# Performance work log

Measured on AMD Instinct MI355X. Metric: run time of the kernel, lower is better.

The kernel has to match this reference:

```python
import jax, jax.numpy as jnp
import numpy as np
from jax import lax

B, L, C = 8, 1024, 256
H = 8  # num_heads
EPS = 1e-5


def _conv_bn(img, w, gamma, beta):
    # img: [B, C_in, h, w]; w: [C_out, C_in, 3, 3]; 3x3 conv, stride 1, pad 1, no bias
    out = lax.conv_general_dilated(img, w, window_strides=(1, 1),
                                   padding=[(1, 1), (1, 1)],
                                   dimension_numbers=('NCHW', 'OIHW', 'NCHW'))
    # BatchNorm2d in train mode: per-channel batch stats over (B, h, w), biased var
    mu = out.mean(axis=(0, 2, 3), keepdims=True)
    var = out.var(axis=(0, 2, 3), keepdims=True)
    out = (out - mu) * lax.rsqrt(var + EPS)
    out = out * gamma[None, :, None, None] + beta[None, :, None, None]
    b, c, hh, ww = out.shape
    return out.reshape(b, c, hh * ww).transpose(0, 2, 1)  # b (h w) c


def setup_inputs() -> dict:
    key = jax.random.key(0)
    ks = jax.random.split(key, 10)
    s = 0.02
    inp = {
        'x': jax.random.normal(ks[0], (B, L, C), jnp.float32),
        'y': jax.random.normal(ks[1], (B, L, C), jnp.float32),
        'h': 32,
        'w': 32,
        'conv_q_w': jax.random.normal(ks[2], (C, C, 3, 3), jnp.float32) * s,
        'bn_q_g': jnp.ones((C,), jnp.float32),
        'bn_q_b': jnp.zeros((C,), jnp.float32),
        'conv_k_w': jax.random.normal(ks[3], (C, C, 3, 3), jnp.float32) * s,
        'bn_k_g': jnp.ones((C,), jnp.float32),
        'bn_k_b': jnp.zeros((C,), jnp.float32),
        'conv_v_w': jax.random.normal(ks[4], (C, C, 3, 3), jnp.float32) * s,
        'bn_v_g': jnp.ones((C,), jnp.float32),
        'bn_v_b': jnp.zeros((C,), jnp.float32),
        'Wq': jax.random.normal(ks[5], (C, C), jnp.float32) * s,
        'Wk': jax.random.normal(ks[6], (C, C), jnp.float32) * s,
        'Wv': jax.random.normal(ks[7], (C, C), jnp.float32) * s,
        'Wo': jax.random.normal(ks[8], (C, C), jnp.float32) * s,
        'bo': jnp.zeros((C,), jnp.float32),
    }
    return inp


def reference(x, y, h, w,
              conv_q_w, bn_q_g, bn_q_b,
              conv_k_w, bn_k_g, bn_k_b,
              conv_v_w, bn_v_g, bn_v_b,
              Wq, Wk, Wv, Wo, bo):
    b, t, c = x.shape
    x_img = x.transpose(0, 2, 1).reshape(b, c, h, w)
    y_img = y.transpose(0, 2, 1).reshape(b, c, h, w)

    q = _conv_bn(x_img, conv_q_w, bn_q_g, bn_q_b)  # [B, L, C]
    k = _conv_bn(y_img, conv_k_w, bn_k_g, bn_k_b)
    v = _conv_bn(y_img, conv_v_w, bn_v_g, bn_v_b)

    d = c // H
    # Linear (no bias) then split heads: b t (h d) -> b h t d
    q = (q @ Wq.T).reshape(b, -1, H, d).transpose(0, 2, 1, 3)
    k = (k @ Wk.T).reshape(b, -1, H, d).transpose(0, 2, 1, 3)
    v = (v @ Wv.T).reshape(b, -1, H, d).transpose(0, 2, 1, 3)

    scale = c ** (-0.5)  # NOTE: original scales by dim_q**-0.5, not head_dim
    attn = jax.nn.softmax(jnp.einsum('bhlk,bhtk->bhlt', q, k) * scale, axis=-1)
    out = jnp.einsum('bhlt,bhtv->bhlv', attn, v)
    out = out.transpose(0, 2, 1, 3).reshape(b, -1, c)  # b h t d -> b t (h d)
    return out @ Wo.T + bo
```

## Files before the change

### kernel.cpp

```cpp
#include <hip/hip_runtime.h>
#include <cmath>

#define BB 8
#define LLEN 1024
#define CC 256
#define NH 8
#define HD 32
#define IMG 32
#define EPSBN 1e-5f
#define QSCALE 0.0625f
#define SCLOG2E 0.09016844005556f

typedef short bf16x8 __attribute__((ext_vector_type(8)));
typedef short bf16x4 __attribute__((ext_vector_type(4)));
typedef float f32x4 __attribute__((ext_vector_type(4)));

static __device__ __forceinline__ unsigned short f2bf(float v) {
  union { float f; unsigned u; } a; a.f = v;
  unsigned r = a.u + 0x7fff + ((a.u >> 16) & 1);
  return (unsigned short)(r >> 16);
}
static __device__ __forceinline__ float bf2f(unsigned short s) {
  union { unsigned u; float f; } a; a.u = ((unsigned)s) << 16; return a.f;
}

__global__ __launch_bounds__(256) void k_prep(const float* __restrict__ x,
                                              const float* __restrict__ y,
                                              const float* __restrict__ w0,
                                              const float* __restrict__ w1,
                                              const float* __restrict__ w2,
                                              const float* __restrict__ Wo,
                                              short* __restrict__ xh,
                                              short* __restrict__ yh,
                                              short* __restrict__ Wrh,
                                              short* __restrict__ Woh,
                                              short* __restrict__ Wol) {
  int bid = blockIdx.x;
  if (bid < 4096) {
    const float* s = bid >= 2048 ? y : x;
    short* d = bid >= 2048 ? yh : xh;
    size_t i = (size_t)((bid & 2047) << 8) + threadIdx.x;
    float4 v = ((const float4*)s)[i];
    bf16x4 o;
    o[0] = (short)f2bf(v.x); o[1] = (short)f2bf(v.y);
    o[2] = (short)f2bf(v.z); o[3] = (short)f2bf(v.w);
    *(bf16x4*)(d + i * 4) = o;
  } else if (bid < 4864) {
    int k = bid - 4096;
    int t = k >> 8, co = k & 255, ci = threadIdx.x;
    const float* w = t == 0 ? w0 : (t == 1 ? w1 : w2);
    const float* src = w + ((size_t)co * CC + ci) * 9;
    size_t ob = (size_t)t * 9 * 65536;
#pragma unroll
    for (int tap = 0; tap < 9; ++tap)
      Wrh[ob + (size_t)(tap * CC + co) * CC + ci] = (short)f2bf(src[tap]);
  } else {
    int i = ((bid - 4864) << 8) + threadIdx.x;
    float v = Wo[i];
    unsigned short h = f2bf(v);
    Woh[i] = (short)h;
    Wol[i] = (short)f2bf(v - bf2f(h));
  }
}

__global__ __launch_bounds__(256, 3) void k_conv(const short* __restrict__ xh,
                                                 const short* __restrict__ yh,
                                                 const short* __restrict__ Wrh,
                                                 short* __restrict__ ch,
                                                 float* __restrict__ st) {
  __shared__ __align__(16) short sI[340 * 32];
  __shared__ float sws[4][64];
  __shared__ float swq[4][64];

  int tid = threadIdx.x;
  int co0 = blockIdx.x << 6;
  int r0 = blockIdx.y << 3;
  int z = blockIdx.z;
  int t = z >> 3, b = z & 7;
  const short* inb = (t == 0 ? xh : yh) + (size_t)b * LLEN * CC;
  const short* wb = Wrh + (size_t)t * 9 * 65536;

  int lane = tid & 63, w = tid >> 6;
  int quad = lane >> 4, mm = lane & 15;

  int pbA[4];
#pragma unroll
  for (int mt = 0; mt < 4; ++mt) {
    int sp = w * 64 + mt * 16 + mm;
    pbA[mt] = (sp >> 5) * 34 + (sp & 31);
  }
  const int dtap[9] = {0, 1, 2, 34, 35, 36, 68, 69, 70};

  const short* wbase = wb + (size_t)(co0 + mm) * CC + quad * 8;

  f32x4 acc[4][4];
#pragma unroll
  for (int mt = 0; mt < 4; ++mt)
#pragma unroll
    for (int nt = 0; nt < 4; ++nt) acc[mt][nt] = (f32x4){0.f, 0.f, 0.f, 0.f};

  for (int kc = 0; kc < 8; ++kc) {
    int ci0 = kc << 5;
    __syncthreads();
#pragma unroll
    for (int j = 0; j < 6; ++j) {
      int idx = tid + (j << 8);
      if (idx < 1360) {
        int sp_p = idx >> 2, cg = idx & 3;
        int pr = sp_p / 34;
        int px = sp_p - pr * 34;
        int ir = r0 - 1 + pr;
        int xx = px - 1;
        bf16x8 v = {0, 0, 0, 0, 0, 0, 0, 0};
        if (ir >= 0 && ir < IMG && xx >= 0 && xx < IMG)
          v = *(const bf16x8*)(inb + (size_t)(ir * 32 + xx) * CC + ci0 + cg * 8);
        *(bf16x8*)(sI + sp_p * 32 + ((cg ^ (sp_p & 3)) << 3)) = v;
      }
    }
    __syncthreads();

    const short* wk0 = wbase + ci0;
#pragma unroll
    for (int tap = 0; tap < 9; ++tap) {
      bf16x8 Bw[4];
#pragma unroll
      for (int nt = 0; nt < 4; ++nt)
        Bw[nt] = *(const bf16x8*)(wk0 + (size_t)tap * 65536 + nt * 4096);
      bf16x8 Af[4];
#pragma unroll
      for (int mt = 0; mt < 4; ++mt) {
        int sp_p = pbA[mt] + dtap[tap];
        Af[mt] = *(const bf16x8*)(sI + sp_p * 32 + ((quad ^ (sp_p & 3)) << 3));
      }
#pragma unroll
      for (int mt = 0; mt < 4; ++mt)
#pragma unroll
        for (int nt = 0; nt < 4; ++nt)
          acc[mt][nt] = __builtin_amdgcn_mfma_f32_16x16x32_bf16(Af[mt], Bw[nt],
                                                                acc[mt][nt], 0, 0, 0);
    }
  }

  size_t tb = (size_t)t * 8192 + b * 1024 + r0 * 32;
#pragma unroll
  for (int mt = 0; mt < 4; ++mt)
#pragma unroll
    for (int nt = 0; nt < 4; ++nt)
#pragma unroll
      for (int r = 0; r < 4; ++r) {
        int sp = w * 64 + mt * 16 + quad * 4 + r;
        ch[(tb + sp) * CC + co0 + nt * 16 + mm] = (short)f2bf(acc[mt][nt][r]);
      }

  float s[4], q[4];
#pragma unroll
  for (int nt = 0; nt < 4; ++nt) {
    float ss = 0.f, qq = 0.f;
#pragma unroll
    for (int mt = 0; mt < 4; ++mt)
#pragma unroll
      for (int r = 0; r < 4; ++r) {
        float v = acc[mt][nt][r];
        ss += v;
        qq += v * v;
      }
    ss += __shfl_xor(ss, 16); ss += __shfl_xor(ss, 32);
    qq += __shfl_xor(qq, 16); qq += __shfl_xor(qq, 32);
    s[nt] = ss; q[nt] = qq;
  }
  if (quad == 0) {
#pragma unroll
    for (int nt = 0; nt < 4; ++nt) {
      sws[w][nt * 16 + mm] = s[nt];
      swq[w][nt * 16 + mm] = q[nt];
    }
  }
  __syncthreads();
  if (tid < 64) {
    float S = sws[0][tid] + sws[1][tid] + sws[2][tid] + sws[3][tid];
    float Q = swq[0][tid] + swq[1][tid] + swq[2][tid] + swq[3][tid];
    atomicAdd(&st[t * 512 + co0 + tid], S);
    atomicAdd(&st[t * 512 + 256 + co0 + tid], Q);
  }
}

__global__ __launch_bounds__(256) void k_fuse(const float* __restrict__ Wq,
                                              const float* __restrict__ Wk,
                                              const float* __restrict__ Wv,
                                              const float* __restrict__ gq,
                                              const float* __restrict__ gk,
                                              const float* __restrict__ gv,
                                              const float* __restrict__ bq,
                                              const float* __restrict__ bk,
                                              const float* __restrict__ bv,
                                              const float* __restrict__ st,
                                              short* __restrict__ Wfh,
                                              short* __restrict__ Wfl,
                                              float* __restrict__ bfv) {
  int t = blockIdx.y;
  const float* W = t == 0 ? Wq : (t == 1 ? Wk : Wv);
  const float* gamma = t == 0 ? gq : (t == 1 ? gk : gv);
  const float* beta = t == 0 ? bq : (t == 1 ? bk : bv);
  int co = blockIdx.x, ci = threadIdx.x;
  float mu = st[t * 512 + ci] * (1.f / 8192.f);
  float var = st[t * 512 + 256 + ci] * (1.f / 8192.f) - mu * mu;
  float a = gamma[ci] * rsqrtf(var + EPSBN);
  float dt = beta[ci] - mu * a;
  float wv = W[co * CC + ci];
  float v = wv * a;
  unsigned short hh = f2bf(v);
  Wfh[(size_t)t * 65536 + co * CC + ci] = (short)hh;
  Wfl[(size_t)t * 65536 + co * CC + ci] = (short)f2bf(v - bf2f(hh));
  __shared__ float red[256];
  red[ci] = dt * wv;
  __syncthreads();
  for (int s2 = 128; s2 > 0; s2 >>= 1) {
    if (ci < s2) red[ci] += red[ci + s2];
    __syncthreads();
  }
  if (ci == 0) bfv[t * 256 + co] = red[0];
}

__global__ __launch_bounds__(256, 2) void k_proj(const short* __restrict__ ch,
                                                 const short* __restrict__ Wfh,
                                                 const short* __restrict__ Wfl,
                                                 const float* __restrict__ bfv,
                                                 short* __restrict__ Qh,
                                                 short* __restrict__ Kh,
                                                 short* __restrict__ Vh) {
  __shared__ __align__(16) short sT[64 * 264];
  int tid = threadIdx.x;
  int t = blockIdx.z;
  int t0 = blockIdx.x << 8;
  int co0 = blockIdx.y << 6;
  int lane = tid & 63, w = tid >> 6;
  int quad = lane >> 4, mm = lane & 15;
  int colw = co0 + w * 16;
  const short* cht = ch + (size_t)t * 8192 * CC;

  bf16x8 Bh[8], Bl[8];
  {
    const short* bh = Wfh + (size_t)t * 65536 + (size_t)(colw + mm) * CC + quad * 8;
    const short* bl = Wfl + (size_t)t * 65536 + (size_t)(colw + mm) * CC + quad * 8;
#pragma unroll
    for (int kc = 0; kc < 8; ++kc) {
      Bh[kc] = *(const bf16x8*)(bh + kc * 32);
      Bl[kc] = *(const bf16x8*)(bl + kc * 32);
    }
  }
  float bv = bfv[t * 256 + colw + mm];

  bf16x8 A0[8], A1[8];
  auto loadA = [&](bf16x8* dst, int g) {
    const short* a = cht + (size_t)(t0 + g * 16 + mm) * CC + quad * 8;
#pragma unroll
    for (int kc = 0; kc < 8; ++kc) dst[kc] = *(const bf16x8*)(a + kc * 32);
  };
  auto compute = [&](const bf16x8* A, int g) {
    f32x4 aH = {0.f, 0.f, 0.f, 0.f}, aL = {0.f, 0.f, 0.f, 0.f};
#pragma unroll
    for (int kc = 0; kc < 8; ++kc) {
      aH = __builtin_amdgcn_mfma_f32_16x16x32_bf16(A[kc], Bh[kc], aH, 0, 0, 0);
      aL = __builtin_amdgcn_mfma_f32_16x16x32_bf16(A[kc], Bl[kc], aL, 0, 0, 0);
    }
    if (t == 0) {
#pragma unroll
      for (int r = 0; r < 4; ++r) {
        int token = t0 + g * 16 + quad * 4 + r;
        Qh[(size_t)token * CC + colw + mm] =
            (short)f2bf((aH[r] + aL[r] + bv) * SCLOG2E);
      }
    } else if (t == 1) {
#pragma unroll
      for (int r = 0; r < 4; ++r) {
        int token = t0 + g * 16 + quad * 4 + r;
        Kh[(size_t)token * CC + colw + mm] = (short)f2bf(aH[r] + aL[r] + bv);
      }
    } else {
#pragma unroll
      for (int r = 0; r < 4; ++r)
        sT[(w * 16 + mm) * 264 + (g >> 2) * 64 + 16 * quad + 4 * r + (g & 3)] =
            (short)f2bf(aH[r] + aL[r] + bv);
    }
  };

  loadA(A0, 0);
#pragma unroll
  for (int g = 0; g < 16; g += 2) {
    loadA(A1, g + 1);
    compute(A0, g);
    if (g + 2 < 16) loadA(A0, g + 2);
    compute(A1, g + 1);
  }

  if (t == 2) {
    __syncthreads();
    int b = t0 >> 10, l0 = t0 & 1023;
#pragma unroll
    for (int j = 0; j < 8; ++j) {
      int idx = tid + (j << 8);
      int co = idx >> 5, tg = idx & 31;
      bf16x8 v = *(const bf16x8*)(sT + co * 264 + tg * 8);
      *(bf16x8*)(Vh + ((size_t)(b * CC) + co0 + co) * LLEN + l0 + tg * 8) = v;
    }
  }
}

__global__ __launch_bounds__(256, 2) void k_attn(const short* __restrict__ Qh,
                                                 const short* __restrict__ Kh,
                                                 const short* __restrict__ Vh,
                                                 short* __restrict__ AOh) {
  __shared__ __align__(16) short sK[2][64 * 32];
  __shared__ __align__(16) short sV[2][32 * 72];
  __shared__ __align__(16) short sP[4 * 32 * 72];

  int tid = threadIdx.x;
  int lane = tid & 63, w = tid >> 6;
  int quad = lane >> 4, mm = lane & 15;
  int bh = blockIdx.x;
  int b = bh >> 3, h = bh & 7;
  int l0 = blockIdx.y << 7;

  bf16x8 qf[2];
#pragma unroll
  for (int mf = 0; mf < 2; ++mf)
    qf[mf] = *(const bf16x8*)(Qh + ((size_t)(b * LLEN) + l0 + w * 32 + mf * 16 + mm) * CC +
                              h * HD + quad * 8);

  f32x4 accO[2][2], accL[2];
#pragma unroll
  for (int mf = 0; mf < 2; ++mf) {
    accO[mf][0] = (f32x4){0.f, 0.f, 0.f, 0.f};
    accO[mf][1] = (f32x4){0.f, 0.f, 0.f, 0.f};
    accL[mf] = (f32x4){0.f, 0.f, 0.f, 0.f};
  }
  bf16x8 ones;
#pragma unroll
  for (int j = 0; j < 8; ++j) ones[j] = (short)0x3F80;

  int kt = tid >> 2, kc4 = tid & 3;
  const short* kgp = Kh + ((size_t)(b * LLEN) + kt) * CC + h * HD + kc4 * 8;
  int kofs = kt * 32 + kc4 * 8;
  int vd = tid >> 3, vt8 = tid & 7;
  const short* vgp = Vh + ((size_t)(b * CC) + h * HD + vd) * LLEN + vt8 * 8;
  int vofs = vd * 72 + vt8 * 8;
  short* pw = sP + w * (32 * 72);

  bf16x8 kr = *(const bf16x8*)kgp;
  bf16x8 vr = *(const bf16x8*)vgp;
  *(bf16x8*)(sK[0] + kofs) = kr;
  *(bf16x8*)(sV[0] + vofs) = vr;
  __syncthreads();

  for (int tt = 0; tt < 16; ++tt) {
    if (tt < 15) {
      kr = *(const bf16x8*)(kgp + (size_t)(tt + 1) * 64 * CC);
      vr = *(const bf16x8*)(vgp + (tt + 1) * 64);
    }
    const short* sKc = sK[tt & 1];
    const short* sVc = sV[tt & 1];

#pragma unroll
    for (int mf = 0; mf < 2; ++mf) {
      f32x4 accS[4];
#pragma unroll
      for (int nt = 0; nt < 4; ++nt) {
        bf16x8 kf = *(const bf16x8*)(sKc + (nt * 16 + mm) * 32 + quad * 8);
        f32x4 z = {0.f, 0.f, 0.f, 0.f};
        accS[nt] = __builtin_amdgcn_mfma_f32_16x16x32_bf16(qf[mf], kf, z, 0, 0, 0);
      }
#pragma unroll
      for (int r = 0; r < 4; ++r) {
        int q = mf * 16 + quad * 4 + r;
        bf16x4 pk;
#pragma unroll
        for (int nt = 0; nt < 4; ++nt) {
          union { float f; unsigned u; } cv;
          cv.f = __builtin_exp2f(accS[nt][r]);
          pk[nt] = (short)((cv.u + 0x8000u) >> 16);
        }
        *(bf16x4*)(pw + q * 72 + mm * 4) = pk;
      }
    }

#pragma unroll
    for (int kc = 0; kc < 2; ++kc) {
      bf16x8 vf0 = *(const bf16x8*)(sVc + mm * 72 + kc * 32 + quad * 8);
      bf16x8 vf1 = *(const bf16x8*)(sVc + (16 + mm) * 72 + kc * 32 + quad * 8);
#pragma unroll
      for (int mf = 0; mf < 2; ++mf) {
        bf16x8 pf = *(const bf16x8*)(pw + (mf * 16 + mm) * 72 + kc * 32 + quad * 8);
        accL[mf] = __builtin_amdgcn_mfma_f32_16x16x32_bf16(pf, ones, accL[mf], 0, 0, 0);
        accO[mf][0] = __builtin_amdgcn_mfma_f32_16x16x32_bf16(pf, vf0, accO[mf][0], 0, 0, 0);
        accO[mf][1] = __builtin_amdgcn_mfma_f32_16x16x32_bf16(pf, vf1, accO[mf][1], 0, 0, 0);
      }
    }

    if (tt < 15) {
      __syncthreads();
      *(bf16x8*)(sK[(tt + 1) & 1] + kofs) = kr;
      *(bf16x8*)(sV[(tt + 1) & 1] + vofs) = vr;
      __syncthreads();
    }
  }

#pragma unroll
  for (int mf = 0; mf < 2; ++mf)
#pragma unroll
    for (int r = 0; r < 4; ++r) {
      float inv = __builtin_amdgcn_rcpf(accL[mf][r]);
      size_t token = (size_t)(b * LLEN) + l0 + w * 32 + mf * 16 + quad * 4 + r;
      AOh[token * CC + h * HD + mm] = (short)f2bf(accO[mf][0][r] * inv);
      AOh[token * CC + h * HD + 16 + mm] = (short)f2bf(accO[mf][1][r] * inv);
    }
}

__global__ __launch_bounds__(256, 2) void k_out(const short* __restrict__ AOh,
                                                const short* __restrict__ Woh,
                                                const short* __restrict__ Wol,
                                                const float* __restrict__ bo,
                                                float* __restrict__ out) {
  int tid = threadIdx.x;
  int t0 = blockIdx.x << 7;
  int co0 = blockIdx.y << 6;
  int lane = tid & 63, w = tid >> 6;
  int quad = lane >> 4, mm = lane & 15;
  int colw = co0 + w * 16;

  bf16x8 Bh[8], Bl[8];
  {
    const short* bh = Woh + (size_t)(colw + mm) * CC + quad * 8;
    const short* bl = Wol + (size_t)(colw + mm) * CC + quad * 8;
#pragma unroll
    for (int kc = 0; kc < 8; ++kc) {
      Bh[kc] = *(const bf16x8*)(bh + kc * 32);
      Bl[kc] = *(const bf16x8*)(bl + kc * 32);
    }
  }
  float bv = bo[colw + mm];

  bf16x8 A0[8], A1[8];
  auto loadA = [&](bf16x8* dst, int g) {
    const short* a = AOh + (size_t)(t0 + g * 16 + mm) * CC + quad * 8;
#pragma unroll
    for (int kc = 0; kc < 8; ++kc) dst[kc] = *(const bf16x8*)(a + kc * 32);
  };
  auto compute = [&](const bf16x8* A, int g) {
    f32x4 aH = {0.f, 0.f, 0.f, 0.f}, aL = {0.f, 0.f, 0.f, 0.f};
#pragma unroll
    for (int kc = 0; kc < 8; ++kc) {
      aH = __builtin_amdgcn_mfma_f32_16x16x32_bf16(A[kc], Bh[kc], aH, 0, 0, 0);
      aL = __builtin_amdgcn_mfma_f32_16x16x32_bf16(A[kc], Bl[kc], aL, 0, 0, 0);
    }
#pragma unroll
    for (int r = 0; r < 4; ++r) {
      int token = t0 + g * 16 + quad * 4 + r;
      out[(size_t)token * CC + colw + mm] = aH[r] + aL[r] + bv;
    }
  };

  loadA(A0, 0);
#pragma unroll
  for (int g = 0; g < 8; g += 2) {
    loadA(A1, g + 1);
    compute(A0, g);
    if (g + 2 < 8) loadA(A0, g + 2);
    compute(A1, g + 1);
  }
}

extern "C" void kernel_launch(void* const* d_in, const int* in_sizes, int n_in,
                              void* d_out, int out_size, void* d_ws, size_t ws_size,
                              hipStream_t stream) {
  (void)in_sizes; (void)n_in; (void)out_size; (void)ws_size;
  const float* x  = (const float*)d_in[0];
  const float* y  = (const float*)d_in[1];
  const float* wq = (const float*)d_in[4];
  const float* gq = (const float*)d_in[5];
  const float* bq = (const float*)d_in[6];
  const float* wk = (const float*)d_in[7];
  const float* gk = (const float*)d_in[8];
  const float* bk = (const float*)d_in[9];
  const float* wv = (const float*)d_in[10];
  const float* gv = (const float*)d_in[11];
  const float* bv = (const float*)d_in[12];
  const float* Wq = (const float*)d_in[13];
  const float* Wk = (const float*)d_in[14];
  const float* Wv = (const float*)d_in[15];
  const float* Wo = (const float*)d_in[16];
  const float* bo = (const float*)d_in[17];
  float* out = (float*)d_out;

  const size_t NP = (size_t)8192 * 256;
  short* xh  = (short*)d_ws;
  short* yh  = xh + NP;
  short* ch  = yh + NP;
  short* Qh  = ch + 3 * NP;
  short* Kh  = Qh + NP;
  short* Vh  = Kh + NP;
  short* AOh = Vh + NP;
  short* Wrh = AOh + NP;
  short* Wfh = Wrh + (size_t)3 * 9 * 65536;
  short* Wfl = Wfh + 3 * 65536;
  short* Woh = Wfl + 3 * 65536;
  short* Wol = Woh + 65536;
  float* st  = (float*)(Wol + 65536);
  float* bfv = st + 1536;

  hipMemsetAsync(st, 0, 1536 * sizeof(float), stream);

  k_prep<<<5120, 256, 0, stream>>>(x, y, wq, wk, wv, Wo, xh, yh, Wrh, Woh, Wol);

  k_conv<<<dim3(4, 4, 24), 256, 0, stream>>>(xh, yh, Wrh, ch, st);

  k_fuse<<<dim3(256, 3), 256, 0, stream>>>(Wq, Wk, Wv, gq, gk, gv, bq, bk, bv,
                                           st, Wfh, Wfl, bfv);

  k_proj<<<dim3(32, 4, 3), 256, 0, stream>>>(ch, Wfh, Wfl, bfv, Qh, Kh, Vh);

  k_attn<<<dim3(64, 8), 256, 0, stream>>>(Qh, Kh, Vh, AOh);

  k_out<<<dim3(64, 4), 256, 0, stream>>>(AOh, Woh, Wol, bo, out);
}
```

Measured before the change: 255.9 us.

## Prepack conv weights per lane, halve conv tile, prefetch inputs, head-major Q/K

Conv weights are repacked in the prep kernel into a per-lane MFMA fragment layout, so each wave reads its B operand contiguously. The conv kernel now covers 4 image rows per block instead of 8, which doubles the grid for more parallelism. It also register-prefetches the next channel chunk of input and double-buffers the weight fragments across taps. Q and K are written head-major so the attention kernel loads contiguous 32-wide rows, and the K shared tile is padded to 40 to avoid bank conflicts. Smaller conv tiles mean more redundant halo loads and more atomic stat updates.

```diff
diff --git a/kernel.cpp b/kernel.cpp
--- a/kernel.cpp
+++ b/kernel.cpp
@@ -32,7 +32,7 @@
                                               const float* __restrict__ Wo,
                                               short* __restrict__ xh,
                                               short* __restrict__ yh,
-                                              short* __restrict__ Wrh,
+                                              short* __restrict__ Wp,
                                               short* __restrict__ Woh,
                                               short* __restrict__ Wol) {
   int bid = blockIdx.x;
@@ -50,10 +50,13 @@
     int t = k >> 8, co = k & 255, ci = threadIdx.x;
     const float* w = t == 0 ? w0 : (t == 1 ? w1 : w2);
     const float* src = w + ((size_t)co * CC + ci) * 9;
-    size_t ob = (size_t)t * 9 * 65536;
+    int cb = co >> 6, nt = (co >> 4) & 3, mmw = co & 15;
+    int kcw = ci >> 5, quadw = (ci >> 3) & 3, e = ci & 7;
+    int lanew = quadw * 16 + mmw;
+    size_t base = ((size_t)(t * 4 + cb) * 8 + kcw) * 9;
 #pragma unroll
     for (int tap = 0; tap < 9; ++tap)
-      Wrh[ob + (size_t)(tap * CC + co) * CC + ci] = (short)f2bf(src[tap]);
+      Wp[((base + tap) * 4 + nt) * 512 + lanew * 8 + e] = (short)f2bf(src[tap]);
   } else {
     int i = ((bid - 4864) << 8) + threadIdx.x;
     float v = Wo[i];
@@ -65,90 +68,116 @@
 
 __global__ __launch_bounds__(256, 3) void k_conv(const short* __restrict__ xh,
                                                  const short* __restrict__ yh,
-                                                 const short* __restrict__ Wrh,
+                                                 const short* __restrict__ Wp,
                                                  short* __restrict__ ch,
                                                  float* __restrict__ st) {
-  __shared__ __align__(16) short sI[340 * 32];
+  __shared__ __align__(16) short sI[204 * 32];
   __shared__ float sws[4][64];
   __shared__ float swq[4][64];
 
   int tid = threadIdx.x;
-  int co0 = blockIdx.x << 6;
-  int r0 = blockIdx.y << 3;
+  int cb = blockIdx.x;
+  int co0 = cb << 6;
+  int r0 = blockIdx.y << 2;
   int z = blockIdx.z;
   int t = z >> 3, b = z & 7;
   const short* inb = (t == 0 ? xh : yh) + (size_t)b * LLEN * CC;
-  const short* wb = Wrh + (size_t)t * 9 * 65536;
 
   int lane = tid & 63, w = tid >> 6;
   int quad = lane >> 4, mm = lane & 15;
 
-  int pbA[4];
-#pragma unroll
-  for (int mt = 0; mt < 4; ++mt) {
-    int sp = w * 64 + mt * 16 + mm;
+  int pbA[2];
+#pragma unroll
+  for (int mt = 0; mt < 2; ++mt) {
+    int sp = w * 32 + mt * 16 + mm;
     pbA[mt] = (sp >> 5) * 34 + (sp & 31);
   }
   const int dtap[9] = {0, 1, 2, 34, 35, 36, 68, 69, 70};
 
-  const short* wbase = wb + (size_t)(co0 + mm) * CC + quad * 8;
-
-  f32x4 acc[4][4];
-#pragma unroll
-  for (int mt = 0; mt < 4; ++mt)
+  bool ivalid[4], iact[4];
+  int ioff[4], sidx[4];
+#pragma unroll
+  for (int j = 0; j < 4; ++j) {
+    int idx = tid + (j << 8);
+    ivalid[j] = idx < 816;
+    int sp_p = idx >> 2, cg = idx & 3;
+    int pr = sp_p / 34;
+    int px = sp_p - pr * 34;
+    int ir = r0 - 1 + pr;
+    int xx = px - 1;
+    iact[j] = ivalid[j] && (ir >= 0) && (ir < IMG) && (xx >= 0) && (xx < IMG);
+    ioff[j] = ((ir < 0 ? 0 : ir) * 32 + (xx < 0 ? 0 : (xx > 31 ? 31 : xx))) * CC + cg * 8;
+    sidx[j] = sp_p * 32 + (((cg + (sp_p >> 1)) & 3) << 3);
+  }
+
+  const short* wlane = Wp + ((size_t)(t * 4 + cb) * 8 * 9 * 4) * 512 + lane * 8;
+
+  f32x4 acc[2][4];
+#pragma unroll
+  for (int mt = 0; mt < 2; ++mt)
 #pragma unroll
     for (int nt = 0; nt < 4; ++nt) acc[mt][nt] = (f32x4){0.f, 0.f, 0.f, 0.f};
 
+  bf16x8 zerov = {0, 0, 0, 0, 0, 0, 0, 0};
+  bf16x8 ipf[4];
+#pragma unroll
+  for (int j = 0; j < 4; ++j)
+    ipf[j] = iact[j] ? *(const bf16x8*)(inb + ioff[j]) : zerov;
+
+  bf16x8 Bw[2][4];
+#pragma unroll
+  for (int nt = 0; nt < 4; ++nt)
+    Bw[0][nt] = *(const bf16x8*)(wlane + (size_t)nt * 512);
+
+  int pb = 0;
   for (int kc = 0; kc < 8; ++kc) {
     int ci0 = kc << 5;
     __syncthreads();
 #pragma unroll
-    for (int j = 0; j < 6; ++j) {
-      int idx = tid + (j << 8);
-      if (idx < 1360) {
-        int sp_p = idx >> 2, cg = idx & 3;
-        int pr = sp_p / 34;
-        int px = sp_p - pr * 34;
-        int ir = r0 - 1 + pr;
-        int xx = px - 1;
-        bf16x8 v = {0, 0, 0, 0, 0, 0, 0, 0};
-        if (ir >= 0 && ir < IMG && xx >= 0 && xx < IMG)
-          v = *(const bf16x8*)(inb + (size_t)(ir * 32 + xx) * CC + ci0 + cg * 8);
-        *(bf16x8*)(sI + sp_p * 32 + ((cg ^ (sp_p & 3)) << 3)) = v;
-      }
-    }
+    for (int j = 0; j < 4; ++j)
+      if (ivalid[j]) *(bf16x8*)(sI + sidx[j]) = ipf[j];
     __syncthreads();
-
-    const short* wk0 = wbase + ci0;
+    if (kc < 7) {
+#pragma unroll
+      for (int j = 0; j < 4; ++j)
+        ipf[j] = iact[j] ? *(const bf16x8*)(inb + ioff[j] + ci0 + 32) : zerov;
+    }
+
 #pragma unroll
     for (int tap = 0; tap < 9; ++tap) {
-      bf16x8 Bw[4];
-#pragma unroll
-      for (int nt = 0; nt < 4; ++nt)
-        Bw[nt] = *(const bf16x8*)(wk0 + (size_t)tap * 65536 + nt * 4096);
-      bf16x8 Af[4];
-#pragma unroll
-      for (int mt = 0; mt < 4; ++mt) {
+      int nb = pb ^ 1;
+      if (!(kc == 7 && tap == 8)) {
+        int nkc = (tap == 8) ? kc + 1 : kc;
+        int ntap = (tap == 8) ? 0 : tap + 1;
+        size_t fo = (size_t)((nkc * 9 + ntap) * 4) * 512;
+#pragma unroll
+        for (int nt = 0; nt < 4; ++nt)
+          Bw[nb][nt] = *(const bf16x8*)(wlane + fo + (size_t)nt * 512);
+      }
+      bf16x8 Af[2];
+#pragma unroll
+      for (int mt = 0; mt < 2; ++mt) {
         int sp_p = pbA[mt] + dtap[tap];
-        Af[mt] = *(const bf16x8*)(sI + sp_p * 32 + ((quad ^ (sp_p & 3)) << 3));
-      }
-#pragma unroll
-      for (int mt = 0; mt < 4; ++mt)
+        Af[mt] = *(const bf16x8*)(sI + sp_p * 32 + (((quad + (sp_p >> 1)) & 3) << 3));
+      }
+#pragma unroll
+      for (int mt = 0; mt < 2; ++mt)
 #pragma unroll
         for (int nt = 0; nt < 4; ++nt)
-          acc[mt][nt] = __builtin_amdgcn_mfma_f32_16x16x32_bf16(Af[mt], Bw[nt],
+          acc[mt][nt] = __builtin_amdgcn_mfma_f32_16x16x32_bf16(Af[mt], Bw[pb][nt],
                                                                 acc[mt][nt], 0, 0, 0);
+      pb = nb;
     }
   }
 
   size_t tb = (size_t)t * 8192 + b * 1024 + r0 * 32;
 #pragma unroll
-  for (int mt = 0; mt < 4; ++mt)
+  for (int mt = 0; mt < 2; ++mt)
 #pragma unroll
     for (int nt = 0; nt < 4; ++nt)
 #pragma unroll
       for (int r = 0; r < 4; ++r) {
-        int sp = w * 64 + mt * 16 + quad * 4 + r;
+        int sp = w * 32 + mt * 16 + quad * 4 + r;
         ch[(tb + sp) * CC + co0 + nt * 16 + mm] = (short)f2bf(acc[mt][nt][r]);
       }
 
@@ -157,7 +186,7 @@
   for (int nt = 0; nt < 4; ++nt) {
     float ss = 0.f, qq = 0.f;
 #pragma unroll
-    for (int mt = 0; mt < 4; ++mt)
+    for (int mt = 0; mt < 2; ++mt)
 #pragma unroll
       for (int r = 0; r < 4; ++r) {
         float v = acc[mt][nt][r];
@@ -250,6 +279,11 @@
   }
   float bv = bfv[t * 256 + colw + mm];
 
+  int c = colw + mm;
+  int hh = c >> 5, dd = c & 31;
+  int bb = t0 >> 10, lbase = t0 & 1023;
+  size_t hb = (size_t)(bb * 8 + hh) * 1024;
+
   bf16x8 A0[8], A1[8];
   auto loadA = [&](bf16x8* dst, int g) {
     const short* a = cht + (size_t)(t0 + g * 16 + mm) * CC + quad * 8;
@@ -266,15 +300,14 @@
     if (t == 0) {
 #pragma unroll
       for (int r = 0; r < 4; ++r) {
-        int token = t0 + g * 16 + quad * 4 + r;
-        Qh[(size_t)token * CC + colw + mm] =
-            (short)f2bf((aH[r] + aL[r] + bv) * SCLOG2E);
+        int l = lbase + g * 16 + quad * 4 + r;
+        Qh[(hb + l) * 32 + dd] = (short)f2bf((aH[r] + aL[r] + bv) * SCLOG2E);
       }
     } else if (t == 1) {
 #pragma unroll
       for (int r = 0; r < 4; ++r) {
-        int token = t0 + g * 16 + quad * 4 + r;
-        Kh[(size_t)token * CC + colw + mm] = (short)f2bf(aH[r] + aL[r] + bv);
+        int l = lbase + g * 16 + quad * 4 + r;
+        Kh[(hb + l) * 32 + dd] = (short)f2bf(aH[r] + aL[r] + bv);
       }
     } else {
 #pragma unroll
@@ -310,7 +343,7 @@
                                                  const short* __restrict__ Kh,
                                                  const short* __restrict__ Vh,
                                                  short* __restrict__ AOh) {
-  __shared__ __align__(16) short sK[2][64 * 32];
+  __shared__ __align__(16) short sK[2][64 * 40];
   __shared__ __align__(16) short sV[2][32 * 72];
   __shared__ __align__(16) short sP[4 * 32 * 72];
 
@@ -324,8 +357,8 @@
   bf16x8 qf[2];
 #pragma unroll
   for (int mf = 0; mf < 2; ++mf)
-    qf[mf] = *(const bf16x8*)(Qh + ((size_t)(b * LLEN) + l0 + w * 32 + mf * 16 + mm) * CC +
-                              h * HD + quad * 8);
+    qf[mf] = *(const bf16x8*)(Qh + ((size_t)bh * 1024 + l0 + w * 32 + mf * 16 + mm) * 32 +
+                              quad * 8);
 
   f32x4 accO[2][2], accL[2];
 #pragma unroll
@@ -339,8 +372,8 @@
   for (int j = 0; j < 8; ++j) ones[j] = (short)0x3F80;
 
   int kt = tid >> 2, kc4 = tid & 3;
-  const short* kgp = Kh + ((size_t)(b * LLEN) + kt) * CC + h * HD + kc4 * 8;
-  int kofs = kt * 32 + kc4 * 8;
+  const short* kgp = Kh + ((size_t)bh * 1024 + kt) * 32 + kc4 * 8;
+  int kofs = kt * 40 + kc4 * 8;
   int vd = tid >> 3, vt8 = tid & 7;
   const short* vgp = Vh + ((size_t)(b * CC) + h * HD + vd) * LLEN + vt8 * 8;
   int vofs = vd * 72 + vt8 * 8;
@@ -354,7 +387,7 @@
 
   for (int tt = 0; tt < 16; ++tt) {
     if (tt < 15) {
-      kr = *(const bf16x8*)(kgp + (size_t)(tt + 1) * 64 * CC);
+      kr = *(const bf16x8*)(kgp + (size_t)(tt + 1) * 64 * 32);
       vr = *(const bf16x8*)(vgp + (tt + 1) * 64);
     }
     const short* sKc = sK[tt & 1];
@@ -365,7 +398,7 @@
       f32x4 accS[4];
 #pragma unroll
       for (int nt = 0; nt < 4; ++nt) {
-        bf16x8 kf = *(const bf16x8*)(sKc + (nt * 16 + mm) * 32 + quad * 8);
+        bf16x8 kf = *(const bf16x8*)(sKc + (nt * 16 + mm) * 40 + quad * 8);
         f32x4 z = {0.f, 0.f, 0.f, 0.f};
         accS[nt] = __builtin_amdgcn_mfma_f32_16x16x32_bf16(qf[mf], kf, z, 0, 0, 0);
       }
@@ -499,8 +532,8 @@
   short* Kh  = Qh + NP;
   short* Vh  = Kh + NP;
   short* AOh = Vh + NP;
-  short* Wrh = AOh + NP;
-  short* Wfh = Wrh + (size_t)3 * 9 * 65536;
+  short* Wp  = AOh + NP;
+  short* Wfh = Wp + (size_t)3 * 9 * 65536;
   short* Wfl = Wfh + 3 * 65536;
   short* Woh = Wfl + 3 * 65536;
   short* Wol = Woh + 65536;
@@ -509,9 +542,9 @@
 
   hipMemsetAsync(st, 0, 1536 * sizeof(float), stream);
 
-  k_prep<<<5120, 256, 0, stream>>>(x, y, wq, wk, wv, Wo, xh, yh, Wrh, Woh, Wol);
-
-  k_conv<<<dim3(4, 4, 24), 256, 0, stream>>>(xh, yh, Wrh, ch, st);
+  k_prep<<<5120, 256, 0, stream>>>(x, y, wq, wk, wv, Wo, xh, yh, Wp, Woh, Wol);
+
+  k_conv<<<dim3(4, 8, 24), 256, 0, stream>>>(xh, yh, Wp, ch, st);
 
   k_fuse<<<dim3(256, 3), 256, 0, stream>>>(Wq, Wk, Wv, gq, gk, gv, bq, bk, bv,
                                            st, Wfh, Wfl, bfv);
```

After: 217.8 us. 14.9% less time.
